# Performance work log

Hardware: AMD Instinct MI355X
Metric: run time of the kernel (lower is better)

## Reference

```python
import jax, jax.numpy as jnp
import numpy as np

D_MODEL = 1024
N_HEADS = 16
D_HEAD = D_MODEL // N_HEADS
BATCH = 2
SEQ = 2048


def setup_inputs() -> dict:
    key = jax.random.key(0)
    ks = jax.random.split(key, 16)
    s = 0.02
    d = D_MODEL
    return {
        "x": jax.random.normal(ks[0], (BATCH, SEQ, d), jnp.float32),
        "Wq": jax.random.normal(ks[1], (d, d), jnp.float32) * s,
        "bq": jnp.zeros((d,), jnp.float32),
        "Wk": jax.random.normal(ks[2], (d, d), jnp.float32) * s,
        "bk": jnp.zeros((d,), jnp.float32),
        "Wv": jax.random.normal(ks[3], (d, d), jnp.float32) * s,
        "bv": jnp.zeros((d,), jnp.float32),
        "Wo": jax.random.normal(ks[4], (d, d), jnp.float32) * s,
        "bo": jnp.zeros((d,), jnp.float32),
        "Wt": jax.random.normal(ks[5], (d, 1), jnp.float32) * s,
        "bt": jnp.zeros((1,), jnp.float32),
        "Wg": jax.random.normal(ks[6], (d, d), jnp.float32) * s,
        "bg": jnp.zeros((d,), jnp.float32),
    }


def _evolved_attention(x, Wq, bq, Wk, bk, Wv, bv, Wo, bo, Wt, bt, Wg, bg):
    B, S, D = x.shape
    H, dh = N_HEADS, D_HEAD

    def heads(y):  # [B,S,D] -> [B,H,S,dh]
        return y.reshape(B, S, H, dh).transpose(0, 2, 1, 3)

    q = heads(x @ Wq + bq)
    k = heads(x @ Wk + bk)
    v = heads(x @ Wv + bv)

    # cosine similarity (F.normalize with eps=1e-12)
    qn = q / jnp.maximum(jnp.linalg.norm(q, axis=-1, keepdims=True), 1e-12)
    kn = k / jnp.maximum(jnp.linalg.norm(k, axis=-1, keepdims=True), 1e-12)
    scores = jnp.einsum("bhqd,bhkd->bhqk", qn, kn)

    # adaptive temperature: sigmoid(temp_proj(mean_s x)) + 0.5, shape [B,1]
    temp = jax.nn.sigmoid(x.mean(axis=1) @ Wt + bt) + 0.5  # [B,1]
    scores = scores / temp[:, None, None, :]  # broadcast [B,1,1,1]

    # sparsemax-style: softmax over top-k (k = S//4), scattered back
    kk = max(1, S // 4)
    vals, idx = jax.lax.top_k(scores, kk)          # [B,H,S,kk]
    w = jax.nn.softmax(vals, axis=-1)
    rows = jnp.arange(B * H * S)[:, None]
    attn = (
        jnp.zeros((B * H * S, S), scores.dtype)
        .at[rows, idx.reshape(-1, kk)]
        .set(w.reshape(-1, kk))
        .reshape(B, H, S, S)
    )

    out = jnp.einsum("bhqk,bhkd->bhqd", attn, v)
    out = out.transpose(0, 2, 1, 3).reshape(B, S, D)
    out = out @ Wo + bo

    # highway gating
    gate = jax.nn.sigmoid(x @ Wg + bg)
    return gate * out + (1.0 - gate) * x


def reference(x, Wq, bq, Wk, bk, Wv, bv, Wo, bo, Wt, bt, Wg, bg):
    return _evolved_attention(x, Wq, bq, Wk, bk, Wv, bv, Wo, bo, Wt, bt, Wg, bg)
```

## Files before the change

### kernel.cpp

```cpp
#include <hip/hip_runtime.h>

typedef unsigned short u16;
typedef __attribute__((ext_vector_type(4))) float f32x4;
typedef __attribute__((ext_vector_type(8))) short bf16x8;
typedef __attribute__((ext_vector_type(4))) int i32x4;

#define BB 2
#define SS 2048
#define DD 1024
#define HH 16
#define DH 64
#define KK 512

#define OFF_SCAL  ((size_t)0)
#define OFF_WT    ((size_t)256)
#define OFF_XB    (OFF_WT + (size_t)5*1024*1024*2)
#define OFF_AO    OFF_XB
#define OFF_QH    (OFF_XB + (size_t)4096*1024*2)
#define OFF_QN    (OFF_QH + (size_t)4096*4096*2)
#define OFF_KN    (OFF_QN + (size_t)4096*1024*2)
#define OFF_VT    (OFF_KN + (size_t)4096*1024*2)

__device__ __forceinline__ float b2f(u16 u) { return __uint_as_float(((unsigned)u) << 16); }
__device__ __forceinline__ u16 f2b(float f) {
    unsigned u = __float_as_uint(f);
    return (u16)((u + 0x7fffu + ((u >> 16) & 1u)) >> 16);
}

__device__ __forceinline__ void gload16(const u16* g, u16* l) {
    __builtin_amdgcn_global_load_lds(
        (__attribute__((address_space(1))) void*)g,
        (__attribute__((address_space(3))) void*)l, 16, 0, 0);
}

__global__ __launch_bounds__(256) void prep(
        const float* x, const float* Wq, const float* Wk, const float* Wv,
        const float* Wg, const float* Wo, const float* Wt,
        u16* xb, u16* WT, float* accbuf) {
    __shared__ float tile[64][65];
    int bid = blockIdx.x;
    if (bid < 4096) {
        int i = (bid * 256 + threadIdx.x) * 4;
        float4 v = *(const float4*)(x + i);
        u16 r0 = f2b(v.x), r1 = f2b(v.y), r2 = f2b(v.z), r3 = f2b(v.w);
        xb[i] = r0; xb[i + 1] = r1; xb[i + 2] = r2; xb[i + 3] = r3;
    } else if (bid < 5376) {
        int t = bid - 4096;
        int z = t >> 8, xy = t & 255;
        const float* src = (z == 0) ? Wq : (z == 1) ? Wk : (z == 2) ? Wv
                         : (z == 3) ? Wg : Wo;
        u16* dst = WT + (size_t)z * 1024 * 1024;
        int n0 = (xy & 15) * 64, k0 = (xy >> 4) * 64;
        int rbase = threadIdx.x >> 6, c = threadIdx.x & 63;
#pragma unroll
        for (int i = 0; i < 16; i++) {
            int r = i * 4 + rbase;
            tile[r][c] = src[(size_t)(k0 + r) * 1024 + n0 + c];
        }
        __syncthreads();
#pragma unroll
        for (int i = 0; i < 16; i++) {
            int r = i * 4 + rbase;
            dst[(size_t)(n0 + r) * 1024 + k0 + c] = f2b(tile[c][r]);
        }
    } else {
        int t = bid - 5376;
        int b = t >> 7, ch = t & 127;
        float a = 0.f;
        for (int si = 0; si < 16; si++) {
            int s = ch * 16 + si;
            const float* xr = x + ((size_t)(b * SS + s)) * DD;
#pragma unroll
            for (int k = 0; k < 4; k++) {
                int c = threadIdx.x + k * 256;
                a += xr[c] * Wt[c];
            }
        }
        for (int o = 32; o; o >>= 1) a += __shfl_xor(a, o);
        __shared__ float red[4];
        if ((threadIdx.x & 63) == 0) red[threadIdx.x >> 6] = a;
        __syncthreads();
        if (threadIdx.x == 0) atomicAdd(&accbuf[b], red[0] + red[1] + red[2] + red[3]);
    }
}

__global__ __launch_bounds__(256) void gemm_qkvg(
        const u16* X, const u16* WT,
        const float* bq, const float* bk, const float* bv, const float* bg, u16* Qh) {
    __shared__ __align__(16) u16 la[128 * 32];
    __shared__ __align__(16) u16 lb[128 * 32];
    int tid = threadIdx.x, wid = tid >> 6, lane = tid & 63;
    int quad = lane >> 4, ml = lane & 15;
    int lid = blockIdx.y * 32 + blockIdx.x;
    int swz = (lid & 7) * 128 + (lid >> 3);
    int m0 = (swz & 31) * 128, n0 = (swz >> 5) * 128;
    int wr = wid >> 1, wc = wid & 1;

    f32x4 acc[4][4];
#pragma unroll
    for (int i = 0; i < 4; i++)
#pragma unroll
        for (int j = 0; j < 4; j++) acc[i][j] = (f32x4){0.f, 0.f, 0.f, 0.f};

    int t0 = wid * 2, t1 = t0 + 1;
    int r0 = lane >> 2, kp = lane & 3;
    const u16* ga0 = X + (size_t)(m0 + t0 * 16 + r0) * 1024 + kp * 8;
    const u16* ga1 = X + (size_t)(m0 + t1 * 16 + r0) * 1024 + kp * 8;
    const u16* gb0 = WT + (size_t)(n0 + t0 * 16 + r0) * 1024 + kp * 8;
    const u16* gb1 = WT + (size_t)(n0 + t1 * 16 + r0) * 1024 + kp * 8;
    u16* la0 = la + t0 * 512; u16* la1 = la + t1 * 512;
    u16* lb0 = lb + t0 * 512; u16* lb1 = lb + t1 * 512;

    for (int k0 = 0; k0 < 1024; k0 += 32) {
        gload16(ga0 + k0, la0);
        gload16(ga1 + k0, la1);
        gload16(gb0 + k0, lb0);
        gload16(gb1 + k0, lb1);
        __syncthreads();
        bf16x8 af[4], bfr[4];
#pragma unroll
        for (int mi = 0; mi < 4; mi++)
            af[mi] = *(const bf16x8*)&la[(wr * 64 + mi * 16 + ml) * 32 + quad * 8];
#pragma unroll
        for (int ni = 0; ni < 4; ni++)
            bfr[ni] = *(const bf16x8*)&lb[(wc * 64 + ni * 16 + ml) * 32 + quad * 8];
#pragma unroll
        for (int mi = 0; mi < 4; mi++)
#pragma unroll
            for (int ni = 0; ni < 4; ni++)
                acc[mi][ni] = __builtin_amdgcn_mfma_f32_16x16x32_bf16(af[mi], bfr[ni],
                                                                      acc[mi][ni], 0, 0, 0);
        __syncthreads();
    }

#pragma unroll
    for (int mi = 0; mi < 4; mi++)
#pragma unroll
        for (int ni = 0; ni < 4; ni++) {
            int col = n0 + wc * 64 + ni * 16 + ml;
            int mat = col >> 10, bc = col & 1023;
            const float* bp = (mat == 0) ? bq : (mat == 1) ? bk : (mat == 2) ? bv : bg;
            float bias = bp[bc];
#pragma unroll
            for (int r = 0; r < 4; r++) {
                int row = m0 + wr * 64 + mi * 16 + quad * 4 + r;
                Qh[(size_t)row * 4096 + col] = f2b(acc[mi][ni][r] + bias);
            }
        }
}

__global__ __launch_bounds__(256) void norm_repack(const u16* Qh, const float* accbuf,
                                                   const float* bt, float* itemp,
                                                   u16* qn, u16* kn, u16* vt) {
    __shared__ u16 vtile[64][66];
    int bid = blockIdx.x;
    if (bid == 0 && threadIdx.x < BB) {
        float v = accbuf[threadIdx.x] / (float)SS + bt[0];
        float tmp = 1.f / (1.f + __expf(-v)) + 0.5f;
        itemp[threadIdx.x] = 1.f / tmp;
    }
    int bh = bid >> 5, st = bid & 31;
    int b = bh >> 4, h = bh & 15;
    int s0 = st * 64;
    int tid = threadIdx.x, wid = tid >> 6, lane = tid & 63;

    for (int i = 0; i < 16; i++) {
        int tt = i * 4 + wid;
        int s = s0 + tt;
        const u16* rowp = Qh + (size_t)(b * SS + s) * 4096 + h * 64;
        float q = b2f(rowp[lane]);
        float k = b2f(rowp[1024 + lane]);
        u16 v = rowp[2048 + lane];
        float sq = q * q, sk = k * k;
#pragma unroll
        for (int o = 32; o; o >>= 1) { sq += __shfl_xor(sq, o); sk += __shfl_xor(sk, o); }
        float qd = fmaxf(sqrtf(sq), 1e-12f), kd = fmaxf(sqrtf(sk), 1e-12f);
        qn[((size_t)bh * SS + s) * DH + lane] = f2b(q / qd);
        kn[((size_t)bh * SS + s) * DH + lane] = f2b(k / kd);
        vtile[lane][tt] = v;
    }
    __syncthreads();

#pragma unroll
    for (int p = 0; p < 2; p++) {
        int d = p * 32 + wid * 8 + (lane >> 3);
        int sc = lane & 7;
        const u16* src = &vtile[d][sc * 8];
        unsigned w0 = *(const unsigned*)(src);
        unsigned w1 = *(const unsigned*)(src + 2);
        unsigned w2 = *(const unsigned*)(src + 4);
        unsigned w3 = *(const unsigned*)(src + 6);
        i32x4 out4 = (i32x4){(int)w0, (int)w1, (int)w2, (int)w3};
        *(i32x4*)(vt + ((size_t)bh * DH + d) * SS + s0 + sc * 8) = out4;
    }
}

#define EST 2088

__global__ __launch_bounds__(1024, 8) void attn_kernel(
        const u16* qn, const u16* kn, const u16* vt, const float* itemp, u16* ao) {
    __shared__ __align__(16) u16 e16[16 * EST];
    __shared__ float pvp[3][16][66];
    __shared__ float zrow_s[16];

    int tid = threadIdx.x, wid = tid >> 6, lane = tid & 63;
    int quad = lane >> 4, nl = lane & 15;
    int bid = blockIdx.x;
    int swz = (bid & 7) * 512 + (bid >> 3);
    int bh = swz >> 7, qt = swz & 127;
    int b = bh >> 4, h = bh & 15;
    const u16* qbase = qn + ((size_t)bh * SS + qt * 16) * DH;
    const u16* kbase = kn + (size_t)bh * SS * DH;
    const u16* vbase = vt + (size_t)bh * DH * SS;
    float it = itemp[b];

    bf16x8 aq0 = *(const bf16x8*)(qbase + nl * DH + quad * 8);
    bf16x8 aq1 = *(const bf16x8*)(qbase + nl * DH + 32 + quad * 8);

#pragma unroll 4
    for (int c = 0; c < 8; c++) {
        int j = c * 256 + wid * 16 + nl;
        const u16* kr = kbase + (size_t)j * DH;
        bf16x8 b0 = *(const bf16x8*)(kr + quad * 8);
        bf16x8 b1 = *(const bf16x8*)(kr + 32 + quad * 8);
        f32x4 acc = (f32x4){0.f, 0.f, 0.f, 0.f};
        __builtin_amdgcn_s_setprio(1);
        acc = __builtin_amdgcn_mfma_f32_16x16x32_bf16(aq0, b0, acc, 0, 0, 0);
        acc = __builtin_amdgcn_mfma_f32_16x16x32_bf16(aq1, b1, acc, 0, 0, 0);
        __builtin_amdgcn_s_setprio(0);
#pragma unroll
        for (int r = 0; r < 4; r++) e16[(quad * 4 + r) * EST + j] = f2b(acc[r] * it);
    }
    __syncthreads();

    {
        u16* rp = &e16[wid * EST];
        int kk[32];
#pragma unroll
        for (int i = 0; i < 4; i++) {
            i32x4 kv = *(const i32x4*)(rp + i * 512 + lane * 8);
#pragma unroll
            for (int j = 0; j < 4; j++) {
                unsigned r2 = (unsigned)kv[j];
                unsigned t = ((r2 >> 15) & 0x00010001u) * 0x7FFFu;
                unsigned key2 = r2 ^ 0x80008000u ^ t;
                int lo = (int)(key2 & 0xFFFFu), hi = (int)(key2 >> 16);
                asm volatile("v_mov_b32 %0, %1" : "=v"(kk[i * 8 + j * 2]) : "v"(lo));
                asm volatile("v_mov_b32 %0, %1" : "=v"(kk[i * 8 + j * 2 + 1]) : "v"(hi));
            }
        }

        int P = 0;
        for (int bit = 15; bit >= 0; bit--) {
            int cand = P | (1 << bit);
            int c0 = 0, c1 = 0, c2 = 0, c3 = 0;
#pragma unroll
            for (int c = 0; c < 32; c += 4) {
                c0 += (int)__popcll(__ballot(kk[c] >= cand));
                c1 += (int)__popcll(__ballot(kk[c + 1] >= cand));
                c2 += (int)__popcll(__ballot(kk[c + 2] >= cand));
                c3 += (int)__popcll(__ballot(kk[c + 3] >= cand));
            }
            int cnt = (c0 + c1) + (c2 + c3);
            if (cnt >= KK) P = cand;
            if (cnt == KK) break;
        }

        float z = 0.f;
#pragma unroll
        for (int i = 0; i < 4; i++) {
            i32x4 ev;
#pragma unroll
            for (int j = 0; j < 4; j++) {
                int k0i = kk[i * 8 + j * 2], k1i = kk[i * 8 + j * 2 + 1];
                unsigned r0 = (unsigned)k0i ^ ((k0i & 0x8000) ? 0x8000u : 0xFFFFu);
                unsigned r1 = (unsigned)k1i ^ ((k1i & 0x8000) ? 0x8000u : 0xFFFFu);
                float f0 = __uint_as_float(r0 << 16);
                float f1 = __uint_as_float(r1 << 16);
                float e0 = (k0i >= P) ? __expf(f0) : 0.f;
                float e1 = (k1i >= P) ? __expf(f1) : 0.f;
                z += e0 + e1;
                int pw;
                asm("v_cvt_pk_bf16_f32 %0, %1, %2" : "=v"(pw) : "v"(e0), "v"(e1));
                ev[j] = pw;
            }
            *(i32x4*)(rp + i * 512 + lane * 8) = ev;
        }
#pragma unroll
        for (int o = 32; o; o >>= 1) z += __shfl_xor(z, o);
        if (lane == 0) zrow_s[wid] = z;
    }
    __syncthreads();

    f32x4 accp = (f32x4){0.f, 0.f, 0.f, 0.f};
    int kq = wid >> 2, g = wid & 3;
    int dh = g * 16 + nl;
    const u16* vrow = vbase + (size_t)dh * SS;
#pragma unroll 4
    for (int c = 0; c < 8; c++) {
        int j0 = kq * 512 + c * 64;
#pragma unroll
        for (int ks = 0; ks < 2; ks++) {
            bf16x8 a = *(const bf16x8*)&e16[nl * EST + j0 + ks * 32 + quad * 8];
            bf16x8 bfr = *(const bf16x8*)(vrow + j0 + ks * 32 + quad * 8);
            __builtin_amdgcn_s_setprio(1);
            accp = __builtin_amdgcn_mfma_f32_16x16x32_bf16(a, bfr, accp, 0, 0, 0);
            __builtin_amdgcn_s_setprio(0);
        }
    }
    if (kq) {
#pragma unroll
        for (int r = 0; r < 4; r++) pvp[kq - 1][quad * 4 + r][dh] = accp[r];
    }
    __syncthreads();
    if (kq == 0) {
#pragma unroll
        for (int r = 0; r < 4; r++) {
            int q = quad * 4 + r;
            float val = (accp[r] + pvp[0][q][dh] + pvp[1][q][dh] + pvp[2][q][dh]) / zrow_s[q];
            size_t row = (size_t)(b * SS + qt * 16 + q);
            ao[row * DD + h * 64 + dh] = f2b(val);
        }
    }
}

__global__ __launch_bounds__(256) void gemm_out(
        const u16* AO, const u16* WTo, const float* bo,
        const u16* Qh, const float* x, float* out) {
    __shared__ __align__(16) u16 la[128 * 32];
    __shared__ __align__(16) u16 lb[128 * 32];
    int tid = threadIdx.x, wid = tid >> 6, lane = tid & 63;
    int quad = lane >> 4, ml = lane & 15;
    int lid = blockIdx.y * 32 + blockIdx.x;
    int swz = (lid & 7) * 32 + (lid >> 3);
    int m0 = (swz & 31) * 128, n0 = (swz >> 5) * 128;
    int wr = wid >> 1, wc = wid & 1;

    f32x4 acc[4][4];
#pragma unroll
    for (int i = 0; i < 4; i++)
#pragma unroll
        for (int j = 0; j < 4; j++) acc[i][j] = (f32x4){0.f, 0.f, 0.f, 0.f};

    int t0 = wid * 2, t1 = t0 + 1;
    int r0 = lane >> 2, kp = lane & 3;
    const u16* ga0 = AO + (size_t)(m0 + t0 * 16 + r0) * 1024 + kp * 8;
    const u16* ga1 = AO + (size_t)(m0 + t1 * 16 + r0) * 1024 + kp * 8;
    const u16* gb0 = WTo + (size_t)(n0 + t0 * 16 + r0) * 1024 + kp * 8;
    const u16* gb1 = WTo + (size_t)(n0 + t1 * 16 + r0) * 1024 + kp * 8;
    u16* la0 = la + t0 * 512; u16* la1 = la + t1 * 512;
    u16* lb0 = lb + t0 * 512; u16* lb1 = lb + t1 * 512;

    for (int k0 = 0; k0 < 1024; k0 += 32) {
        gload16(ga0 + k0, la0);
        gload16(ga1 + k0, la1);
        gload16(gb0 + k0, lb0);
        gload16(gb1 + k0, lb1);
        __syncthreads();
        bf16x8 af[4], bfr[4];
#pragma unroll
        for (int mi = 0; mi < 4; mi++)
            af[mi] = *(const bf16x8*)&la[(wr * 64 + mi * 16 + ml) * 32 + quad * 8];
#pragma unroll
        for (int ni = 0; ni < 4; ni++)
            bfr[ni] = *(const bf16x8*)&lb[(wc * 64 + ni * 16 + ml) * 32 + quad * 8];
#pragma unroll
        for (int mi = 0; mi < 4; mi++)
#pragma unroll
            for (int ni = 0; ni < 4; ni++)
                acc[mi][ni] = __builtin_amdgcn_mfma_f32_16x16x32_bf16(af[mi], bfr[ni],
                                                                      acc[mi][ni], 0, 0, 0);
        __syncthreads();
    }

#pragma unroll
    for (int mi = 0; mi < 4; mi++)
#pragma unroll
        for (int ni = 0; ni < 4; ni++) {
            int col = n0 + wc * 64 + ni * 16 + ml;
            float bias = bo[col];
#pragma unroll
            for (int r = 0; r < 4; r++) {
                int row = m0 + wr * 64 + mi * 16 + quad * 4 + r;
                float gv = b2f(Qh[(size_t)row * 4096 + 3072 + col]);
                float gate = 1.f / (1.f + __expf(-gv));
                float xv = x[(size_t)row * 1024 + col];
                float o = acc[mi][ni][r] + bias;
                out[(size_t)row * 1024 + col] = gate * o + (1.f - gate) * xv;
            }
        }
}

extern "C" void kernel_launch(void* const* d_in, const int* in_sizes, int n_in,
                              void* d_out, int out_size, void* d_ws, size_t ws_size,
                              hipStream_t stream) {
    const float* x  = (const float*)d_in[0];
    const float* Wq = (const float*)d_in[1];
    const float* bq = (const float*)d_in[2];
    const float* Wk = (const float*)d_in[3];
    const float* bk = (const float*)d_in[4];
    const float* Wv = (const float*)d_in[5];
    const float* bv = (const float*)d_in[6];
    const float* Wo = (const float*)d_in[7];
    const float* bo = (const float*)d_in[8];
    const float* Wt = (const float*)d_in[9];
    const float* bt = (const float*)d_in[10];
    const float* Wg = (const float*)d_in[11];
    const float* bg = (const float*)d_in[12];

    char* w = (char*)d_ws;
    float* accbuf = (float*)(w + OFF_SCAL);
    float* itemp  = accbuf + 2;
    u16*   WT     = (u16*)(w + OFF_WT);
    u16*   xb     = (u16*)(w + OFF_XB);
    u16*   ao     = (u16*)(w + OFF_AO);
    u16*   Qh     = (u16*)(w + OFF_QH);
    u16*   qn     = (u16*)(w + OFF_QN);
    u16*   kn     = (u16*)(w + OFF_KN);
    u16*   vt     = (u16*)(w + OFF_VT);

    hipMemsetAsync(accbuf, 0, 2 * sizeof(float), stream);

    prep<<<5632, 256, 0, stream>>>(x, Wq, Wk, Wv, Wg, Wo, Wt, xb, WT, accbuf);
    gemm_qkvg<<<dim3(32, 32), 256, 0, stream>>>(xb, WT, bq, bk, bv, bg, Qh);
    norm_repack<<<1024, 256, 0, stream>>>(Qh, accbuf, bt, itemp, qn, kn, vt);
    attn_kernel<<<4096, 1024, 0, stream>>>(qn, kn, vt, itemp, ao);
    gemm_out<<<dim3(32, 8), 256, 0, stream>>>(ao, WT + (size_t)4 * 1024 * 1024, bo, Qh, x,
                                              (float*)d_out);
}
```

Measured before the change: 488.4 us.

## Fuse Q/K normalization and V transpose into QKVG GEMM epilogue

The GEMM epilogue now writes normalized Q and K rows directly in head-major layout, and writes V transposed into the vt buffer. L2 norms are reduced with lane shuffles across the 16-lane column group. Only the gate projection still goes to the wide Qh buffer. This removes the separate norm_repack kernel, along with its extra launch and the round trip through Qh. The temperature scalar is now computed inline in the attention kernel. The cost is scattered 2-byte and 8-byte epilogue stores in place of coalesced ones.

```diff
diff --git a/kernel.cpp b/kernel.cpp
--- a/kernel.cpp
+++ b/kernel.cpp
@@ -4,6 +4,7 @@
 typedef __attribute__((ext_vector_type(4))) float f32x4;
 typedef __attribute__((ext_vector_type(8))) short bf16x8;
 typedef __attribute__((ext_vector_type(4))) int i32x4;
+typedef __attribute__((ext_vector_type(4))) unsigned short u16x4;
 
 #define BB 2
 #define SS 2048
@@ -86,7 +87,8 @@
 
 __global__ __launch_bounds__(256) void gemm_qkvg(
         const u16* X, const u16* WT,
-        const float* bq, const float* bk, const float* bv, const float* bg, u16* Qh) {
+        const float* bq, const float* bk, const float* bv, const float* bg,
+        u16* Qh, u16* qn, u16* kn, u16* vt) {
     __shared__ __align__(16) u16 la[128 * 32];
     __shared__ __align__(16) u16 lb[128 * 32];
     int tid = threadIdx.x, wid = tid >> 6, lane = tid & 63;
@@ -133,72 +135,78 @@
         __syncthreads();
     }
 
-#pragma unroll
-    for (int mi = 0; mi < 4; mi++)
-#pragma unroll
-        for (int ni = 0; ni < 4; ni++) {
-            int col = n0 + wc * 64 + ni * 16 + ml;
-            int mat = col >> 10, bc = col & 1023;
-            const float* bp = (mat == 0) ? bq : (mat == 1) ? bk : (mat == 2) ? bv : bg;
-            float bias = bp[bc];
+    int matn = n0 >> 10;
+    int basecol = (n0 & 1023) + wc * 64;
+    int token0 = m0 + wr * 64;
+    int b = token0 >> 11;
+    int h = basecol >> 6;
+    int bh = b * HH + h;
+
+    if (matn == 3) {
+#pragma unroll
+        for (int mi = 0; mi < 4; mi++)
+#pragma unroll
+            for (int ni = 0; ni < 4; ni++) {
+                int col = n0 + wc * 64 + ni * 16 + ml;
+                float bias = bg[col & 1023];
+#pragma unroll
+                for (int r = 0; r < 4; r++) {
+                    int row = m0 + wr * 64 + mi * 16 + quad * 4 + r;
+                    Qh[(size_t)row * 4096 + col] = f2b(acc[mi][ni][r] + bias);
+                }
+            }
+    } else if (matn == 2) {
+        float bias[4];
+#pragma unroll
+        for (int ni = 0; ni < 4; ni++) bias[ni] = bv[basecol + ni * 16 + ml];
+#pragma unroll
+        for (int mi = 0; mi < 4; mi++) {
+            int sb = (token0 + mi * 16 + quad * 4) & 2047;
+#pragma unroll
+            for (int ni = 0; ni < 4; ni++) {
+                int dh = ni * 16 + ml;
+                u16x4 w;
+#pragma unroll
+                for (int r = 0; r < 4; r++) w[r] = f2b(acc[mi][ni][r] + bias[ni]);
+                *(u16x4*)(vt + ((size_t)bh * DH + dh) * SS + sb) = w;
+            }
+        }
+    } else {
+        const float* bp = matn ? bk : bq;
+        u16* dst = matn ? kn : qn;
+        float bias[4];
+#pragma unroll
+        for (int ni = 0; ni < 4; ni++) bias[ni] = bp[basecol + ni * 16 + ml];
+#pragma unroll
+        for (int mi = 0; mi < 4; mi++)
 #pragma unroll
             for (int r = 0; r < 4; r++) {
-                int row = m0 + wr * 64 + mi * 16 + quad * 4 + r;
-                Qh[(size_t)row * 4096 + col] = f2b(acc[mi][ni][r] + bias);
-            }
-        }
-}
-
-__global__ __launch_bounds__(256) void norm_repack(const u16* Qh, const float* accbuf,
-                                                   const float* bt, float* itemp,
-                                                   u16* qn, u16* kn, u16* vt) {
-    __shared__ u16 vtile[64][66];
-    int bid = blockIdx.x;
-    if (bid == 0 && threadIdx.x < BB) {
-        float v = accbuf[threadIdx.x] / (float)SS + bt[0];
-        float tmp = 1.f / (1.f + __expf(-v)) + 0.5f;
-        itemp[threadIdx.x] = 1.f / tmp;
-    }
-    int bh = bid >> 5, st = bid & 31;
-    int b = bh >> 4, h = bh & 15;
-    int s0 = st * 64;
-    int tid = threadIdx.x, wid = tid >> 6, lane = tid & 63;
-
-    for (int i = 0; i < 16; i++) {
-        int tt = i * 4 + wid;
-        int s = s0 + tt;
-        const u16* rowp = Qh + (size_t)(b * SS + s) * 4096 + h * 64;
-        float q = b2f(rowp[lane]);
-        float k = b2f(rowp[1024 + lane]);
-        u16 v = rowp[2048 + lane];
-        float sq = q * q, sk = k * k;
-#pragma unroll
-        for (int o = 32; o; o >>= 1) { sq += __shfl_xor(sq, o); sk += __shfl_xor(sk, o); }
-        float qd = fmaxf(sqrtf(sq), 1e-12f), kd = fmaxf(sqrtf(sk), 1e-12f);
-        qn[((size_t)bh * SS + s) * DH + lane] = f2b(q / qd);
-        kn[((size_t)bh * SS + s) * DH + lane] = f2b(k / kd);
-        vtile[lane][tt] = v;
-    }
-    __syncthreads();
-
-#pragma unroll
-    for (int p = 0; p < 2; p++) {
-        int d = p * 32 + wid * 8 + (lane >> 3);
-        int sc = lane & 7;
-        const u16* src = &vtile[d][sc * 8];
-        unsigned w0 = *(const unsigned*)(src);
-        unsigned w1 = *(const unsigned*)(src + 2);
-        unsigned w2 = *(const unsigned*)(src + 4);
-        unsigned w3 = *(const unsigned*)(src + 6);
-        i32x4 out4 = (i32x4){(int)w0, (int)w1, (int)w2, (int)w3};
-        *(i32x4*)(vt + ((size_t)bh * DH + d) * SS + s0 + sc * 8) = out4;
+                float q[4];
+                float ss = 0.f;
+#pragma unroll
+                for (int ni = 0; ni < 4; ni++) {
+                    q[ni] = acc[mi][ni][r] + bias[ni];
+                    ss += q[ni] * q[ni];
+                }
+                ss += __shfl_xor(ss, 1);
+                ss += __shfl_xor(ss, 2);
+                ss += __shfl_xor(ss, 4);
+                ss += __shfl_xor(ss, 8);
+                float rn = 1.f / fmaxf(sqrtf(ss), 1e-12f);
+                int s = (token0 + mi * 16 + quad * 4 + r) & 2047;
+                u16* rowp = dst + ((size_t)bh * SS + s) * DH;
+#pragma unroll
+                for (int ni = 0; ni < 4; ni++)
+                    rowp[ni * 16 + ml] = f2b(q[ni] * rn);
+            }
     }
 }
 
 #define EST 2088
 
 __global__ __launch_bounds__(1024, 8) void attn_kernel(
-        const u16* qn, const u16* kn, const u16* vt, const float* itemp, u16* ao) {
+        const u16* qn, const u16* kn, const u16* vt,
+        const float* accbuf, const float* bt, u16* ao) {
     __shared__ __align__(16) u16 e16[16 * EST];
     __shared__ float pvp[3][16][66];
     __shared__ float zrow_s[16];
@@ -212,7 +220,9 @@
     const u16* qbase = qn + ((size_t)bh * SS + qt * 16) * DH;
     const u16* kbase = kn + (size_t)bh * SS * DH;
     const u16* vbase = vt + (size_t)bh * DH * SS;
-    float it = itemp[b];
+    float av = accbuf[b] * (1.f / (float)SS) + bt[0];
+    float tmp = 1.f / (1.f + __expf(-av)) + 0.5f;
+    float it = 1.f / tmp;
 
     bf16x8 aq0 = *(const bf16x8*)(qbase + nl * DH + quad * 8);
     bf16x8 aq1 = *(const bf16x8*)(qbase + nl * DH + 32 + quad * 8);
@@ -410,7 +420,6 @@
 
     char* w = (char*)d_ws;
     float* accbuf = (float*)(w + OFF_SCAL);
-    float* itemp  = accbuf + 2;
     u16*   WT     = (u16*)(w + OFF_WT);
     u16*   xb     = (u16*)(w + OFF_XB);
     u16*   ao     = (u16*)(w + OFF_AO);
@@ -422,9 +431,8 @@
     hipMemsetAsync(accbuf, 0, 2 * sizeof(float), stream);
 
     prep<<<5632, 256, 0, stream>>>(x, Wq, Wk, Wv, Wg, Wo, Wt, xb, WT, accbuf);
-    gemm_qkvg<<<dim3(32, 32), 256, 0, stream>>>(xb, WT, bq, bk, bv, bg, Qh);
-    norm_repack<<<1024, 256, 0, stream>>>(Qh, accbuf, bt, itemp, qn, kn, vt);
-    attn_kernel<<<4096, 1024, 0, stream>>>(qn, kn, vt, itemp, ao);
+    gemm_qkvg<<<dim3(32, 32), 256, 0, stream>>>(xb, WT, bq, bk, bv, bg, Qh, qn, kn, vt);
+    attn_kernel<<<4096, 1024, 0, stream>>>(qn, kn, vt, accbuf, bt, ao);
     gemm_out<<<dim3(32, 8), 256, 0, stream>>>(ao, WT + (size_t)4 * 1024 * 1024, bo, Qh, x,
                                               (float*)d_out);
 }
```

New measurement: 483.5 us, median of 2. Within noise of the previous version (-1.0%).
